# Optimization experiments

Measured on AMD Instinct MI355X. Metric: run time of the kernel, lower is better.

Reference implementation:

```python
import jax, jax.numpy as jnp
import numpy as np
from functools import lru_cache

SEG_GROUPS = 2          # len(segment_lengths) = len([1024, 2048])
HEAD_DIM = 64
SCALE = HEAD_DIM ** -0.5


@lru_cache(maxsize=None)
def _hilbert_perm(n: int):
    """Replicates _generate_hilbert_indices. For n a perfect power of 4 this is a
    true permutation (and its inverse)."""
    dim = 1
    while dim * dim < n:
        dim *= 2
    idxs = []
    for i in range(min(n, dim * dim)):
        x = y = 0
        s = 1
        t = i
        while s < dim:
            rx = 1 & (t // 2)
            ry = 1 & (t ^ rx)
            if ry == 0:
                if rx == 1:
                    x, y = dim and (s - 1 - y), (s - 1 - x)
                x, y = y, x
            x += s * rx
            y += s * ry
            t //= 4
            s *= 2
        cell = x * dim + y
        if cell < n:
            idxs.append(cell)
    if len(idxs) < n:
        idxs.extend(range(len(idxs), n))
    hil = np.asarray(idxs[:n], dtype=np.int64)
    inv = np.zeros(n, dtype=np.int64)
    inv[hil] = np.arange(n, dtype=np.int64)
    return hil, inv


def setup_inputs() -> dict:
    key = jax.random.key(0)
    k1, k2, k3 = jax.random.split(key, 3)
    shape = (4, 4096, 16, 64)  # [batch, seq_len, num_heads, head_dim]
    return {
        "q": jax.random.normal(k1, shape, dtype=jnp.float32),
        "k": jax.random.normal(k2, shape, dtype=jnp.float32),
        "v": jax.random.normal(k3, shape, dtype=jnp.float32),
    }


def reference(q, k, v):
    """Faithful translation of RingDilatedAttentionHilbertOptimizedFixed.forward
    with is_causal=False, dropout=0, dilation_rates=[1,1].

    Fidelity notes:
    - The torch code matmuls [B, L, h, d] @ [B, L, d, h] WITHOUT moving heads to a
      batch dim, so scores are [B, L, h, h]: per-position head-vs-head attention.
      With dilation_rate=1 this makes the segment loop a pure partition of the
      sequence, so we vectorize over the whole (Hilbert-ordered) sequence.
    - Hilbert gather on q/k/v and inverse scatter on the output are kept.
    """
    B, S, H, D = q.shape
    hil_np, inv_np = _hilbert_perm(S)
    hil = jnp.asarray(hil_np)
    inv = jnp.asarray(inv_np)

    # Hilbert-curve reordering along the sequence axis.
    qo = jnp.take(q, hil, axis=1)
    ko = jnp.take(k, hil, axis=1)
    vo = jnp.take(v, hil, axis=1)

    hg = max(1, H // SEG_GROUPS)  # heads_per_segment
    outs = []
    for g in range(SEG_GROUPS):
        hs, he = g * hg, min(g * hg + hg, H)
        qs, ks, vs = qo[:, :, hs:he], ko[:, :, hs:he], vo[:, :, hs:he]
        # per-position head-vs-head scores: [B, S, hg, hg]
        scores = jnp.einsum("bsid,bsjd->bsij", qs, ks) * SCALE
        attn = jax.nn.softmax(scores, axis=-1)
        attn = jnp.nan_to_num(attn, nan=0.0)
        outs.append(jnp.einsum("bsij,bsjd->bsid", attn, vs))
    out = jnp.concatenate(outs, axis=2)  # heads fully covered: 2 * 8 = 16

    # Inverse Hilbert reordering.
    return jnp.take(out, inv, axis=1)
```

## Files before the change

### kernel.cpp

```cpp
#include <hip/hip_runtime.h>
#include <math.h>


#define HEADS 16
#define DIM 64
#define ROWP 68
#define POS_PER_BLOCK 2

__global__ void hilbert_attn_kernel(const float* __restrict__ q,
                                    const float* __restrict__ k,
                                    const float* __restrict__ v,
                                    float* __restrict__ out,
                                    int npos)
{
    __shared__ float sq[POS_PER_BLOCK][HEADS][ROWP];
    __shared__ float sk[POS_PER_BLOCK][HEADS][ROWP];
    __shared__ float sv[POS_PER_BLOCK][HEADS][ROWP];

    const int t = threadIdx.x;
    const long long blockPos = (long long)blockIdx.x * POS_PER_BLOCK;

    {
        const int fo  = t * 4;
        const int row = fo >> 6;
        const int col = fo & 63;
        for (int p = 0; p < POS_PER_BLOCK; ++p) {
            long long pos = blockPos + p;
            if (pos >= npos) break;
            const long long gbase = pos * (HEADS * DIM) + fo;
            float4 a = *(const float4*)(q + gbase);
            float4 b = *(const float4*)(k + gbase);
            float4 c = *(const float4*)(v + gbase);
            *(float4*)&sq[p][row][col] = a;
            *(float4*)&sk[p][row][col] = b;
            *(float4*)&sv[p][row][col] = c;
        }
    }
    __syncthreads();

    const int p    = t >> 7;
    const int tt   = t & 127;
    const int i    = tt >> 3;
    const int j    = tt & 7;
    const int grp  = i >> 3;
    const int lane = t & 63;

    if (blockPos + p >= npos) return;

    float acc = 0.f;
    const int krow = grp * 8 + j;
    #pragma unroll
    for (int d = 0; d < DIM; d += 4) {
        float4 a = *(const float4*)&sq[p][i][d];
        float4 b = *(const float4*)&sk[p][krow][d];
        acc += a.x * b.x + a.y * b.y + a.z * b.z + a.w * b.w;
    }
    float s = acc * 0.125f;

    float m = s;
    #pragma unroll
    for (int off = 1; off < 8; off <<= 1)
        m = fmaxf(m, __shfl_xor(m, off));
    float e = __expf(s - m);
    float sum = e;
    #pragma unroll
    for (int off = 1; off < 8; off <<= 1)
        sum += __shfl_xor(sum, off);
    const float attn = e / sum;

    const int col = j * 8;
    float o0 = 0.f, o1 = 0.f, o2 = 0.f, o3 = 0.f;
    float o4 = 0.f, o5 = 0.f, o6 = 0.f, o7 = 0.f;
    const int vbase = grp * 8;
    #pragma unroll
    for (int jj = 0; jj < 8; ++jj) {
        float a = __shfl(attn, (lane & 56) | jj);
        const float4* vp = (const float4*)&sv[p][vbase + jj][col];
        float4 v0 = vp[0], v1 = vp[1];
        o0 += a * v0.x; o1 += a * v0.y; o2 += a * v0.z; o3 += a * v0.w;
        o4 += a * v1.x; o5 += a * v1.y; o6 += a * v1.z; o7 += a * v1.w;
    }

    const long long gaddr = (blockPos + p) * (HEADS * DIM) + i * DIM + col;
    *(float4*)(out + gaddr)     = make_float4(o0, o1, o2, o3);
    *(float4*)(out + gaddr + 4) = make_float4(o4, o5, o6, o7);
}

extern "C" void kernel_launch(void* const* d_in, const int* in_sizes, int n_in,
                              void* d_out, int out_size, void* d_ws, size_t ws_size,
                              hipStream_t stream) {
    const float* q = (const float*)d_in[0];
    const float* k = (const float*)d_in[1];
    const float* v = (const float*)d_in[2];
    float* out = (float*)d_out;

    const int npos = in_sizes[0] / (HEADS * DIM);
    const int blocks = (npos + POS_PER_BLOCK - 1) / POS_PER_BLOCK;
    hilbert_attn_kernel<<<blocks, 256, 0, stream>>>(q, k, v, out, npos);
}
```

Measured before the change: 218.7 us.

## Map one wavefront per position with per-wave LDS and no block barrier

Restructures the kernel so each 64-lane wavefront handles one sequence position. Each lane owns one query head and a quarter of the head dimension, loads q straight into registers, and stages only K/V in a private padded LDS slice. The block-wide __syncthreads is dropped and the wave's lanes are relied on to see each other's LDS writes. Scores are reduced with two xor shuffles and softmax runs entirely in registers. The aim is to cut LDS traffic, barrier cost and shuffles, at the cost of more registers per thread and a reliance on wave-level ordering of LDS accesses.

```diff
diff --git a/kernel.cpp b/kernel.cpp
--- a/kernel.cpp
+++ b/kernel.cpp
@@ -4,86 +4,107 @@
 
 #define HEADS 16
 #define DIM 64
-#define ROWP 68
-#define POS_PER_BLOCK 2
+#define GSTRIDE 516
+#define TSLICE  (2 * GSTRIDE)
+#define WSLICE  (2 * TSLICE)
+#define WAVES_PER_BLOCK 4
 
-__global__ void hilbert_attn_kernel(const float* __restrict__ q,
-                                    const float* __restrict__ k,
-                                    const float* __restrict__ v,
-                                    float* __restrict__ out,
-                                    int npos)
+__global__ void __launch_bounds__(256) hilbert_attn_kernel(
+    const float* __restrict__ q,
+    const float* __restrict__ k,
+    const float* __restrict__ v,
+    float* __restrict__ out,
+    int npos)
 {
-    __shared__ float sq[POS_PER_BLOCK][HEADS][ROWP];
-    __shared__ float sk[POS_PER_BLOCK][HEADS][ROWP];
-    __shared__ float sv[POS_PER_BLOCK][HEADS][ROWP];
+    __shared__ float lds[WAVES_PER_BLOCK * WSLICE];
 
-    const int t = threadIdx.x;
-    const long long blockPos = (long long)blockIdx.x * POS_PER_BLOCK;
+    const int t    = threadIdx.x;
+    const int wave = t >> 6;
+    const int lane = t & 63;
+    const long long pos = (long long)blockIdx.x * WAVES_PER_BLOCK + wave;
+    if (pos >= npos) return;
+
+    float* kk = lds + wave * WSLICE;
+    float* vv = kk + TSLICE;
+
+    const long long gbase = pos * (HEADS * DIM);
+
+    const int i   = lane >> 2;
+    const int s   = lane & 3;
+    const int grp = i >> 3;
+
+    const float* qp = q + gbase + i * DIM + s * 16;
+    float4 q0 = *(const float4*)(qp + 0);
+    float4 q1 = *(const float4*)(qp + 4);
+    float4 q2 = *(const float4*)(qp + 8);
+    float4 q3 = *(const float4*)(qp + 12);
 
     {
-        const int fo  = t * 4;
-        const int row = fo >> 6;
-        const int col = fo & 63;
-        for (int p = 0; p < POS_PER_BLOCK; ++p) {
-            long long pos = blockPos + p;
-            if (pos >= npos) break;
-            const long long gbase = pos * (HEADS * DIM) + fo;
-            float4 a = *(const float4*)(q + gbase);
-            float4 b = *(const float4*)(k + gbase);
-            float4 c = *(const float4*)(v + gbase);
-            *(float4*)&sq[p][row][col] = a;
-            *(float4*)&sk[p][row][col] = b;
-            *(float4*)&sv[p][row][col] = c;
+        #pragma unroll
+        for (int it = 0; it < 4; ++it) {
+            const int sfo = it * 256 + lane * 4;
+            const int dfo = sfo + ((it >= 2) ? 4 : 0);
+            float4 a = *(const float4*)(k + gbase + sfo);
+            float4 b = *(const float4*)(v + gbase + sfo);
+            *(float4*)(kk + dfo) = a;
+            *(float4*)(vv + dfo) = b;
         }
     }
-    __syncthreads();
 
-    const int p    = t >> 7;
-    const int tt   = t & 127;
-    const int i    = tt >> 3;
-    const int j    = tt & 7;
-    const int grp  = i >> 3;
-    const int lane = t & 63;
-
-    if (blockPos + p >= npos) return;
-
-    float acc = 0.f;
-    const int krow = grp * 8 + j;
+    const float* kg = kk + grp * GSTRIDE;
+    float sc[8];
     #pragma unroll
-    for (int d = 0; d < DIM; d += 4) {
-        float4 a = *(const float4*)&sq[p][i][d];
-        float4 b = *(const float4*)&sk[p][krow][d];
-        acc += a.x * b.x + a.y * b.y + a.z * b.z + a.w * b.w;
+    for (int j = 0; j < 8; ++j) {
+        const float* kr = kg + j * DIM + s * 16;
+        float4 k0 = *(const float4*)(kr + 0);
+        float4 k1 = *(const float4*)(kr + 4);
+        float4 k2 = *(const float4*)(kr + 8);
+        float4 k3 = *(const float4*)(kr + 12);
+        float a = q0.x*k0.x + q0.y*k0.y + q0.z*k0.z + q0.w*k0.w
+                + q1.x*k1.x + q1.y*k1.y + q1.z*k1.z + q1.w*k1.w
+                + q2.x*k2.x + q2.y*k2.y + q2.z*k2.z + q2.w*k2.w
+                + q3.x*k3.x + q3.y*k3.y + q3.z*k3.z + q3.w*k3.w;
+        sc[j] = a;
     }
-    float s = acc * 0.125f;
-
-    float m = s;
     #pragma unroll
-    for (int off = 1; off < 8; off <<= 1)
-        m = fmaxf(m, __shfl_xor(m, off));
-    float e = __expf(s - m);
-    float sum = e;
-    #pragma unroll
-    for (int off = 1; off < 8; off <<= 1)
-        sum += __shfl_xor(sum, off);
-    const float attn = e / sum;
-
-    const int col = j * 8;
-    float o0 = 0.f, o1 = 0.f, o2 = 0.f, o3 = 0.f;
-    float o4 = 0.f, o5 = 0.f, o6 = 0.f, o7 = 0.f;
-    const int vbase = grp * 8;
-    #pragma unroll
-    for (int jj = 0; jj < 8; ++jj) {
-        float a = __shfl(attn, (lane & 56) | jj);
-        const float4* vp = (const float4*)&sv[p][vbase + jj][col];
-        float4 v0 = vp[0], v1 = vp[1];
-        o0 += a * v0.x; o1 += a * v0.y; o2 += a * v0.z; o3 += a * v0.w;
-        o4 += a * v1.x; o5 += a * v1.y; o6 += a * v1.z; o7 += a * v1.w;
+    for (int j = 0; j < 8; ++j) {
+        sc[j] += __shfl_xor(sc[j], 1);
+        sc[j] += __shfl_xor(sc[j], 2);
+        sc[j] *= 0.125f;
     }
 
-    const long long gaddr = (blockPos + p) * (HEADS * DIM) + i * DIM + col;
-    *(float4*)(out + gaddr)     = make_float4(o0, o1, o2, o3);
-    *(float4*)(out + gaddr + 4) = make_float4(o4, o5, o6, o7);
+    float m = sc[0];
+    #pragma unroll
+    for (int j = 1; j < 8; ++j) m = fmaxf(m, sc[j]);
+    float sum = 0.f;
+    float at[8];
+    #pragma unroll
+    for (int j = 0; j < 8; ++j) { at[j] = __expf(sc[j] - m); sum += at[j]; }
+    const float inv = 1.f / sum;
+    #pragma unroll
+    for (int j = 0; j < 8; ++j) at[j] *= inv;
+
+    const float* vg = vv + grp * GSTRIDE;
+    float4 o0 = make_float4(0,0,0,0), o1 = o0, o2 = o0, o3 = o0;
+    #pragma unroll
+    for (int j = 0; j < 8; ++j) {
+        const float a = at[j];
+        const float* vr = vg + j * DIM + s * 16;
+        float4 v0 = *(const float4*)(vr + 0);
+        float4 v1 = *(const float4*)(vr + 4);
+        float4 v2 = *(const float4*)(vr + 8);
+        float4 v3 = *(const float4*)(vr + 12);
+        o0.x += a*v0.x; o0.y += a*v0.y; o0.z += a*v0.z; o0.w += a*v0.w;
+        o1.x += a*v1.x; o1.y += a*v1.y; o1.z += a*v1.z; o1.w += a*v1.w;
+        o2.x += a*v2.x; o2.y += a*v2.y; o2.z += a*v2.z; o2.w += a*v2.w;
+        o3.x += a*v3.x; o3.y += a*v3.y; o3.z += a*v3.z; o3.w += a*v3.w;
+    }
+
+    float* op = out + gbase + i * DIM + s * 16;
+    *(float4*)(op + 0)  = o0;
+    *(float4*)(op + 4)  = o1;
+    *(float4*)(op + 8)  = o2;
+    *(float4*)(op + 12) = o3;
 }
 
 extern "C" void kernel_launch(void* const* d_in, const int* in_sizes, int n_in,
@@ -95,6 +116,6 @@
     float* out = (float*)d_out;
 
     const int npos = in_sizes[0] / (HEADS * DIM);
-    const int blocks = (npos + POS_PER_BLOCK - 1) / POS_PER_BLOCK;
+    const int blocks = (npos + WAVES_PER_BLOCK - 1) / WAVES_PER_BLOCK;
     hilbert_attn_kernel<<<blocks, 256, 0, stream>>>(q, k, v, out, npos);
 }
```

New measurement: 210.4 us. 3.8% less time.
